# Kernel tuning notes

Measured on AMD Instinct MI355X. Metric: run time of the kernel, lower is better.

The kernel has to match this reference:

```python
import jax, jax.numpy as jnp
import numpy as np

B, M, C, S, SD, K, H = 32, 448, 384, 512, 128, 8, 8
DH = C // H
EPS = 1e-5
NEG_SLOPE = 0.2


def setup_inputs() -> dict:
    key = jax.random.key(0)
    ks = iter(jax.random.split(key, 32))
    nrm = lambda shape, scale=0.05: (jax.random.normal(next(ks), shape, jnp.float32) * scale)
    inp = {
        'q': jax.random.normal(next(ks), (B, M, C), jnp.float32),
        'coarse': jax.random.normal(next(ks), (B, M, 3), jnp.float32),
        'skeleton': jax.random.normal(next(ks), (B, S, 3), jnp.float32),
        # GraphConv 1: 3 -> 64 (root weight, rel/neighbor weight, bias)
        'gc1_wroot': nrm((3, 64), 0.3), 'gc1_wrel': nrm((3, 64), 0.3), 'gc1_b': jnp.zeros((64,), jnp.float32),
        # GraphConv 2: 64 -> SD
        'gc2_wroot': nrm((64, SD), 0.1), 'gc2_wrel': nrm((64, SD), 0.1), 'gc2_b': jnp.zeros((SD,), jnp.float32),
        # skeleton_projection: SD -> C
        'proj_w': nrm((SD, C), 0.08), 'proj_b': jnp.zeros((C,), jnp.float32),
        # MultiheadAttention (torch layout: in_proj (3C, C), out_proj (C, C))
        'attn_in_w': nrm((3 * C, C), 0.05), 'attn_in_b': jnp.zeros((3 * C,), jnp.float32),
        'attn_out_w': nrm((C, C), 0.05), 'attn_out_b': jnp.zeros((C,), jnp.float32),
        # increase_dim: Conv1d(C,1024,1) + BN(1024) + LeakyReLU + Conv1d(1024,1024,1)
        'inc1_w': nrm((1024, C), 0.05), 'inc1_b': jnp.zeros((1024,), jnp.float32),
        'bn_g': jnp.ones((1024,), jnp.float32), 'bn_b': jnp.zeros((1024,), jnp.float32),
        'bn_m': jnp.zeros((1024,), jnp.float32), 'bn_v': jnp.ones((1024,), jnp.float32),
        'inc2_w': nrm((1024, 1024), 0.03), 'inc2_b': jnp.zeros((1024,), jnp.float32),
        # reduce_map: Linear(C + 1024 + 3, C)
        'red_w': nrm((1024 + C + 3, C), 0.03), 'red_b': jnp.zeros((C,), jnp.float32),
    }
    return inp


def _knn_idx(pts):
    # pts: [B,S,3]; per-batch kNN (self excluded), matching knn_graph(k=K, batch=...)
    d2 = jnp.sum((pts[:, :, None, :] - pts[:, None, :, :]) ** 2, axis=-1)  # [B,S,S]
    d2 = d2 + jnp.eye(S, dtype=pts.dtype)[None] * 1e10                       # mask self
    _, idx = jax.lax.top_k(-d2, K)                                           # [B,S,K]
    return idx


def _graph_conv(x, idx, wroot, wrel, b):
    # GraphConv (PyG, aggr='add'): out_i = x_i Wroot + (sum_{j in N(i)} x_j) Wrel + b
    nb = jax.vmap(lambda f, i: f[i])(x, idx)   # [B,S,K,F]
    agg = nb.sum(axis=2)                       # [B,S,F]
    return x @ wroot + agg @ wrel + b


def reference(q, coarse, skeleton, gc1_wroot, gc1_wrel, gc1_b, gc2_wroot, gc2_wrel, gc2_b,
              proj_w, proj_b, attn_in_w, attn_in_b, attn_out_w, attn_out_b,
              inc1_w, inc1_b, bn_g, bn_b, bn_m, bn_v, inc2_w, inc2_b, red_w, red_b):
    # --- skeleton branch: knn graph + 2-layer GraphConv + max-pool + projection ---
    idx = _knn_idx(skeleton)
    h = _graph_conv(skeleton, idx, gc1_wroot, gc1_wrel, gc1_b)
    h = jax.nn.relu(h)
    h = _graph_conv(h, idx, gc2_wroot, gc2_wrel, gc2_b)        # [B,S,SD]
    proxy = jnp.max(h, axis=1)                                  # [B,SD]
    proxy = proxy @ proj_w + proj_b                             # [B,C]
    kv = jnp.broadcast_to(proxy[:, None, :], (B, M, C))         # expanded proxies

    # --- cross attention (torch nn.MultiheadAttention math) ---
    wq, wk, wv = attn_in_w[:C], attn_in_w[C:2 * C], attn_in_w[2 * C:]
    bq, bk, bv = attn_in_b[:C], attn_in_b[C:2 * C], attn_in_b[2 * C:]
    qh = (q @ wq.T + bq).reshape(B, M, H, DH)
    kh = (kv @ wk.T + bk).reshape(B, M, H, DH)
    vh = (kv @ wv.T + bv).reshape(B, M, H, DH)
    scores = jnp.einsum('bmhd,bnhd->bhmn', qh, kh) / jnp.sqrt(jnp.float32(DH))
    attn = jax.nn.softmax(scores, axis=-1)
    ctx = jnp.einsum('bhmn,bnhd->bmhd', attn, vh).reshape(B, M, C)
    q = ctx @ attn_out_w.T + attn_out_b                         # fused features [B,M,C]

    # --- increase_dim (1x1 conv == matmul) + BN(eval) + LeakyReLU + 1x1 conv ---
    g = jnp.einsum('bmc,oc->bmo', q, inc1_w) + inc1_b           # [B,M,1024]
    g = bn_g * (g - bn_m) * jax.lax.rsqrt(bn_v + EPS) + bn_b
    g = jnp.where(g >= 0, g, NEG_SLOPE * g)
    g = jnp.einsum('bmc,oc->bmo', g, inc2_w) + inc2_b
    global_feature = jnp.max(g, axis=1)                         # [B,1024]

    # --- concat + reduce_map ---
    rebuild = jnp.concatenate([jnp.broadcast_to(global_feature[:, None, :], (B, M, 1024)), q, coarse], axis=-1)
    out = rebuild @ red_w + red_b                               # [B,M,C]
    return out
```

## Files before the change

kernel.cpp:

```cpp
#include <hip/hip_runtime.h>

#define NB 32
#define MM 448
#define CC 384
#define SS 512
#define KNN 8
#define NBLK 512u

#define WS_IDX    0u
#define WS_H1     524288u
#define WS_PMAX   4718592u
#define WS_VV     4980736u
#define WS_Y      5029888u
#define WS_XCAT   5160960u
#define WS_BASEP  5341184u
#define WS_BAR    5390336u

#define AGENT __HIP_MEMORY_SCOPE_AGENT

__device__ __forceinline__ float ldg_f(const float* p) {
  return __hip_atomic_load(p, __ATOMIC_RELAXED, AGENT);
}
__device__ __forceinline__ void stg_f(float* p, float v) {
  __hip_atomic_store(p, v, __ATOMIC_RELAXED, AGENT);
}

__device__ __forceinline__ float wave_sum(float v) {
#pragma unroll
  for (int m = 1; m < 64; m <<= 1) v += __shfl_xor(v, m, 64);
  return v;
}

__device__ __forceinline__ void gbar(unsigned* bar, int phase, int blk) {
  asm volatile("s_waitcnt vmcnt(0)" ::: "memory");
  __syncthreads();
  if (threadIdx.x == 0) {
    __hip_atomic_fetch_add(bar + (blk & 7) * 16, 1u, __ATOMIC_RELAXED, AGENT);
    long spins = 0;
    unsigned tgt = (unsigned)(phase + 1);
    if (blk == 0) {
      unsigned target = NBLK * tgt;
      for (;;) {
        unsigned s = 0;
#pragma unroll
        for (int i = 0; i < 8; i++)
          s += __hip_atomic_load(bar + i * 16, __ATOMIC_RELAXED, AGENT);
        if (s >= target) break;
        __builtin_amdgcn_s_sleep(8);
        if (++spins > (1L << 21)) break;
      }
      __hip_atomic_store(bar + 8 * 16, tgt, __ATOMIC_RELAXED, AGENT);
    } else {
      while (__hip_atomic_load(bar + 8 * 16, __ATOMIC_RELAXED, AGENT) < tgt) {
        __builtin_amdgcn_s_sleep(8);
        if (++spins > (1L << 21)) break;
      }
    }
  }
  __syncthreads();
}

__global__ __launch_bounds__(256) void k_knn_gc1(
    const float* __restrict__ skel,
    const float* __restrict__ w1root, const float* __restrict__ w1rel,
    const float* __restrict__ b1,
    int* __restrict__ idx_ws, float* __restrict__ h1_ws,
    unsigned* __restrict__ bar)
{
  if (blockIdx.x == 0 && threadIdx.x < 9) bar[threadIdx.x * 16] = 0u;

  int b   = blockIdx.x >> 7;
  int grp = blockIdx.x & 127;
  __shared__ __align__(16) float4 sk[SS];
  const float* sb = skel + b * SS * 3;
  for (int t = threadIdx.x; t < SS; t += 256)
    sk[t] = make_float4(sb[t*3+0], sb[t*3+1], sb[t*3+2], 0.f);
  __syncthreads();

  int wave = threadIdx.x >> 6, lane = threadIdx.x & 63;
  int i = grp * 4 + wave;
  float4 pi = sk[i];

  float bd[KNN];
#pragma unroll
  for (int t = 0; t < KNN; t++) {
    int j = lane + (t << 6);
    float4 p = sk[j];
    float d2;
    {
#pragma clang fp contract(off)
      float dx = pi.x - p.x, dy = pi.y - p.y, dz = pi.z - p.z;
      d2 = (dx*dx + dy*dy) + dz*dz;
    }
    bd[t] = (j == i) ? 3e38f : d2;
  }

  int win[KNN];
  int* idx_base = idx_ws + (size_t)(b*SS + i) * KNN;
#pragma unroll
  for (int t = 0; t < KNN; t++) {
    float bestd = bd[0]; int bests = 0;
#pragma unroll
    for (int s = 1; s < KNN; s++)
      if (bd[s] < bestd) { bestd = bd[s]; bests = s; }
    int bestj = lane + (bests << 6);
#pragma unroll
    for (int m = 1; m < 64; m <<= 1) {
      float od = __shfl_xor(bestd, m, 64);
      int   oj = __shfl_xor(bestj, m, 64);
      if (od < bestd || (od == bestd && oj < bestj)) { bestd = od; bestj = oj; }
    }
    win[t] = bestj;
    if (lane == t) idx_base[t] = bestj;
    if ((bestj & 63) == lane) {
      int sl = bestj >> 6;
#pragma unroll
      for (int s = 0; s < KNN; s++) if (s == sl) bd[s] = 3e38f;
    }
  }

  float a0 = 0.f, a1 = 0.f, a2 = 0.f;
#pragma unroll
  for (int t = 0; t < KNN; t++) {
    float4 n = sk[win[t]];
    a0 += n.x; a1 += n.y; a2 += n.z;
  }

  int c = lane;
  float h = b1[c] + pi.x*w1root[c] + pi.y*w1root[64+c] + pi.z*w1root[128+c]
                  + a0*w1rel[c]   + a1*w1rel[64+c]   + a2*w1rel[128+c];
  h = fmaxf(h, 0.f);
  h1_ws[(size_t)(b*SS + i) * 64 + lane] = h;
}

struct CoopArgs {
  const float* h1; const int* idx;
  const float *g2wr, *g2wl, *g2b;
  const float *projw, *projb;
  const float *aiw, *aib, *aow, *aob;
  const float *i1w, *i1b, *bng, *bnb, *bnm, *bnv;
  const float *i2w, *i2b;
  const float *redw, *redb;
  const float* coarse;
  float *pmax, *vv, *y, *xcat, *basep, *out;
  unsigned* bar;
};

__global__ __launch_bounds__(256, 2) void k_fused(CoopArgs a)
{
  __shared__ __align__(16) float smem[9600];
  const int t   = threadIdx.x;
  const int blk = blockIdx.x;

  {
    int b = blk >> 4, chunk = blk & 15;
    int r0 = chunk * 32;
    float* X    = smem;
    float* Wt   = smem + 4128;
    float* mred = smem + 8224;
    int*   nbs  = (int*)(smem + 9248);

    const float* h1b = a.h1 + (size_t)b * SS * 64;
    nbs[t] = a.idx[(b*SS + r0)*KNN + t];
#pragma unroll
    for (int p = 0; p < 8; p++) {
      int idx = t + 256*p;
      int r = idx >> 6, k = idx & 63;
      X[r*129 + k] = h1b[(r0 + r)*64 + k];
    }
    __syncthreads();
#pragma unroll
    for (int p = 0; p < 8; p++) {
      int idx = t + 256*p;
      int r = idx >> 6, k = idx & 63;
      const int* nb = nbs + r*KNN;
      float s = 0.f;
#pragma unroll
      for (int j = 0; j < KNN; j++) s += h1b[nb[j]*64 + k];
      X[r*129 + 64 + k] = s;
    }

    int rg = t >> 5, cgi = t & 31;
    float acc[4][4];
#pragma unroll
    for (int r = 0; r < 4; r++)
#pragma unroll
      for (int u = 0; u < 4; u++) acc[r][u] = 0.f;

    const float* wsrc[4] = { a.g2wr, a.g2wr + 32*128, a.g2wl, a.g2wl + 32*128 };
#pragma unroll 1
    for (int ch = 0; ch < 4; ch++) {
      __syncthreads();
      const float* ws = wsrc[ch];
#pragma unroll
      for (int p = 0; p < 16; p++) {
        int idx = t + 256*p;
        Wt[idx] = ws[idx];
      }
      __syncthreads();
      int kb = ch * 32;
      const float* xr0 = X + (rg*4+0)*129 + kb;
      const float* xr1 = X + (rg*4+1)*129 + kb;
      const float* xr2 = X + (rg*4+2)*129 + kb;
      const float* xr3 = X + (rg*4+3)*129 + kb;
#pragma unroll 4
      for (int k = 0; k < 32; k++) {
        float4 w4 = *(const float4*)(Wt + k*128 + cgi*4);
        float x0 = xr0[k], x1 = xr1[k], x2 = xr2[k], x3 = xr3[k];
        acc[0][0] += x0*w4.x; acc[0][1] += x0*w4.y; acc[0][2] += x0*w4.z; acc[0][3] += x0*w4.w;
        acc[1][0] += x1*w4.x; acc[1][1] += x1*w4.y; acc[1][2] += x1*w4.z; acc[1][3] += x1*w4.w;
        acc[2][0] += x2*w4.x; acc[2][1] += x2*w4.y; acc[2][2] += x2*w4.z; acc[2][3] += x2*w4.w;
        acc[3][0] += x3*w4.x; acc[3][1] += x3*w4.y; acc[3][2] += x3*w4.z; acc[3][3] += x3*w4.w;
      }
    }
#pragma unroll
    for (int u = 0; u < 4; u++)
      mred[rg*128 + cgi*4 + u] =
        fmaxf(fmaxf(acc[0][u], acc[1][u]), fmaxf(acc[2][u], acc[3][u]));
    __syncthreads();
    if (t < 128) {
      float mx = mred[t];
#pragma unroll
      for (int g = 1; g < 8; g++) mx = fmaxf(mx, mred[g*128 + t]);
      stg_f(&a.pmax[(size_t)(b*16 + chunk)*128 + t], mx + a.g2b[t]);
    }
  }
  gbar(a.bar, 0, blk);

  if (blk < 384) {
    int b = blk & 31, og = blk >> 5;
    if (t < 128) {
      float m = -3e38f;
      for (int ch = 0; ch < 16; ch++)
        m = fmaxf(m, ldg_f(&a.pmax[(size_t)(b*16 + ch)*128 + t]));
      smem[t] = m;
    }
    __syncthreads();
    for (int o = t; o < CC; o += 256) {
      float acc = a.projb[o];
      for (int s = 0; s < 128; s++) acc += smem[s] * a.projw[s*CC + o];
      smem[128 + o] = acc;
    }
    __syncthreads();
    const float* xs = smem + 128;
    int wv = t >> 6, lane = t & 63;
    float x0 = xs[lane*6+0], x1 = xs[lane*6+1], x2 = xs[lane*6+2];
    float x3 = xs[lane*6+3], x4 = xs[lane*6+4], x5 = xs[lane*6+5];
#pragma unroll
    for (int u = 0; u < 8; u++) {
      int o = og*32 + wv*8 + u;
      const float* wr = a.aiw + (size_t)(2*CC + o) * CC + lane*6;
      float2 wa = *(const float2*)wr;
      float2 wb = *(const float2*)(wr + 2);
      float2 wc = *(const float2*)(wr + 4);
      float p = wa.x*x0 + wa.y*x1 + wb.x*x2 + wb.y*x3 + wc.x*x4 + wc.y*x5;
      p = wave_sum(p);
      if (lane == 0) stg_f(&a.vv[b*CC + o], a.aib[2*CC + o] + p);
    }
  }
  gbar(a.bar, 1, blk);

  if (blk < 384) {
    int b = blk & 31, og = blk >> 5;
    for (int i = t; i < CC; i += 256) smem[i] = ldg_f(&a.vv[b*CC + i]);
    __syncthreads();
    int wv = t >> 6, lane = t & 63;
    float x0 = smem[lane*6+0], x1 = smem[lane*6+1], x2 = smem[lane*6+2];
    float x3 = smem[lane*6+3], x4 = smem[lane*6+4], x5 = smem[lane*6+5];
#pragma unroll
    for (int u = 0; u < 8; u++) {
      int o = og*32 + wv*8 + u;
      const float* wr = a.aow + (size_t)o * CC + lane*6;
      float2 wa = *(const float2*)wr;
      float2 wb = *(const float2*)(wr + 2);
      float2 wc = *(const float2*)(wr + 4);
      float p = wa.x*x0 + wa.y*x1 + wb.x*x2 + wb.y*x3 + wc.x*x4 + wc.y*x5;
      p = wave_sum(p);
      if (lane == 0) stg_f(&a.xcat[b*1408 + 1024 + o], a.aob[o] + p);
    }
  }
  gbar(a.bar, 2, blk);

  {
    int b = blk >> 4, og = blk & 15;
    int o = og*64 + (t >> 2), qq = t & 3;
    for (int i = t; i < CC; i += 256) smem[i] = ldg_f(&a.xcat[b*1408 + 1024 + i]);
    __syncthreads();
    const float* wr = a.i1w + (size_t)o * CC + qq*96;
    const float* xr = smem + qq*96;
    float acc = 0.f;
#pragma unroll
    for (int kk = 0; kk < 96; kk += 4) {
      float4 w4 = *(const float4*)(wr + kk);
      float4 x4 = *(const float4*)(xr + kk);
      acc += w4.x*x4.x + w4.y*x4.y + w4.z*x4.z + w4.w*x4.w;
    }
    acc += __shfl_xor(acc, 1, 64);
    acc += __shfl_xor(acc, 2, 64);
    if (qq == 0) {
      float v = acc + a.i1b[o];
      float z = a.bng[o] * (v - a.bnm[o]) * rsqrtf(a.bnv[o] + 1e-5f) + a.bnb[o];
      stg_f(&a.y[b*1024 + o], (z >= 0.f) ? z : 0.2f * z);
    }
  }
  gbar(a.bar, 3, blk);

  {
    int b = blk >> 4, og = blk & 15;
    int o = og*64 + (t >> 2), qq = t & 3;
    for (int i = t; i < 1024; i += 256) smem[i] = ldg_f(&a.y[b*1024 + i]);
    __syncthreads();
    const float* wr = a.i2w + (size_t)o * 1024 + qq*256;
    const float* xr = smem + qq*256;
    float acc = 0.f;
#pragma unroll 8
    for (int kk = 0; kk < 256; kk += 4) {
      float4 w4 = *(const float4*)(wr + kk);
      float4 x4 = *(const float4*)(xr + kk);
      acc += w4.x*x4.x + w4.y*x4.y + w4.z*x4.z + w4.w*x4.w;
    }
    acc += __shfl_xor(acc, 1, 64);
    acc += __shfl_xor(acc, 2, 64);
    if (qq == 0) stg_f(&a.xcat[b*1408 + o], acc + a.i2b[o]);
  }
  gbar(a.bar, 4, blk);

  if (blk < 48) {
    int o0 = blk * 8;
    float* xs = smem;
    float* wt = smem + 4128;
    int o4 = t & 1, bb = (t >> 1) & 31, kq = t >> 6;
    float acc0 = 0.f, acc1 = 0.f, acc2 = 0.f, acc3 = 0.f;
#pragma unroll 1
    for (int c0 = 0; c0 < 1408; c0 += 128) {
      __syncthreads();
#pragma unroll
      for (int p = 0; p < 16; p++) {
        int idx = t + 256*p;
        xs[(idx >> 7)*129 + (idx & 127)] =
          ldg_f(&a.xcat[(idx >> 7)*1408 + c0 + (idx & 127)]);
      }
#pragma unroll
      for (int p = 0; p < 4; p++) {
        int idx = t + 256*p;
        wt[idx] = a.redw[(size_t)(c0 + (idx >> 3)) * CC + o0 + (idx & 7)];
      }
      __syncthreads();
      const float* xrow = xs + bb*129 + kq*32;
      const float* wrow = wt + kq*32*8 + o4*4;
#pragma unroll 8
      for (int i = 0; i < 32; i++) {
        float  x  = xrow[i];
        float4 w4 = *(const float4*)(wrow + i*8);
        acc0 += x*w4.x; acc1 += x*w4.y; acc2 += x*w4.z; acc3 += x*w4.w;
      }
    }
    __syncthreads();
    float* red = smem;
    red[t*4+0] = acc0; red[t*4+1] = acc1; red[t*4+2] = acc2; red[t*4+3] = acc3;
    __syncthreads();
    {
      int bb2 = t >> 3, oj = t & 7;
      float s = 0.f;
#pragma unroll
      for (int k2 = 0; k2 < 4; k2++)
        s += red[(k2*64 + bb2*2 + (oj >> 2))*4 + (oj & 3)];
      stg_f(&a.basep[bb2*CC + o0 + oj], s);
    }
  }
  gbar(a.bar, 5, blk);

  {
    int b = blk >> 4, mg = blk & 15;
    for (int i = t; i < CC; i += 256) smem[i] = ldg_f(&a.basep[b*CC + i]);
    __syncthreads();
    const int m0 = mg * 28;
    for (int i = t; i < 28*96; i += 256) {
      int mr = i / 96, c4 = i - mr*96;
      int row = b*MM + m0 + mr;
      int c = c4 * 4;
      float4 p0 = *(const float4*)(smem + c);
      float4 rb = *(const float4*)(a.redb + c);
      const float* cr = a.coarse + (size_t)row * 3;
      float cx = cr[0], cy = cr[1], cz = cr[2];
      float4 w0 = *(const float4*)(a.redw + (size_t)1408*CC + c);
      float4 w1 = *(const float4*)(a.redw + (size_t)1409*CC + c);
      float4 w2 = *(const float4*)(a.redw + (size_t)1410*CC + c);
      float4 o4v;
      o4v.x = p0.x + rb.x + cx*w0.x + cy*w1.x + cz*w2.x;
      o4v.y = p0.y + rb.y + cx*w0.y + cy*w1.y + cz*w2.y;
      o4v.z = p0.z + rb.z + cx*w0.z + cy*w1.z + cz*w2.z;
      o4v.w = p0.w + rb.w + cx*w0.w + cy*w1.w + cz*w2.w;
      *(float4*)(a.out + (size_t)row*CC + c) = o4v;
    }
  }
}

extern "C" void kernel_launch(void* const* d_in, const int* in_sizes, int n_in,
                              void* d_out, int out_size, void* d_ws, size_t ws_size,
                              hipStream_t stream)
{
  (void)in_sizes; (void)n_in; (void)out_size; (void)ws_size;
  const float* coarse = (const float*)d_in[1];
  const float* skel   = (const float*)d_in[2];
  const float* g1wr   = (const float*)d_in[3];
  const float* g1wl   = (const float*)d_in[4];
  const float* g1b    = (const float*)d_in[5];

  char* ws = (char*)d_ws;
  int*      idx_ws = (int*)(ws + WS_IDX);
  float*    h1_ws  = (float*)(ws + WS_H1);
  unsigned* bar    = (unsigned*)(ws + WS_BAR);

  CoopArgs a;
  a.h1    = h1_ws;
  a.idx   = idx_ws;
  a.g2wr  = (const float*)d_in[6];
  a.g2wl  = (const float*)d_in[7];
  a.g2b   = (const float*)d_in[8];
  a.projw = (const float*)d_in[9];
  a.projb = (const float*)d_in[10];
  a.aiw   = (const float*)d_in[11];
  a.aib   = (const float*)d_in[12];
  a.aow   = (const float*)d_in[13];
  a.aob   = (const float*)d_in[14];
  a.i1w   = (const float*)d_in[15];
  a.i1b   = (const float*)d_in[16];
  a.bng   = (const float*)d_in[17];
  a.bnb   = (const float*)d_in[18];
  a.bnm   = (const float*)d_in[19];
  a.bnv   = (const float*)d_in[20];
  a.i2w   = (const float*)d_in[21];
  a.i2b   = (const float*)d_in[22];
  a.redw  = (const float*)d_in[23];
  a.redb  = (const float*)d_in[24];
  a.coarse= coarse;
  a.pmax  = (float*)(ws + WS_PMAX);
  a.vv    = (float*)(ws + WS_VV);
  a.y     = (float*)(ws + WS_Y);
  a.xcat  = (float*)(ws + WS_XCAT);
  a.basep = (float*)(ws + WS_BASEP);
  a.out   = (float*)d_out;
  a.bar   = bar;

  k_knn_gc1<<<4096, 256, 0, stream>>>(skel, g1wr, g1wl, g1b, idx_ws, h1_ws, bar);
  k_fused<<<NBLK, 256, 0, stream>>>(a);
}
```

Baseline: 279.2 us.

## Restructure post-graph matvec phases across fewer blocks with decentralized grid barrier

Reworks the persistent kernel's grid barrier so every block polls the summed counters directly, instead of waiting for block 0 to publish a release flag, and uses thread fences instead of a raw waitcnt. The skeleton projection is now computed once by 32 blocks and stored to a new workspace buffer, replacing the redundant per-block recomputation. The attention V/out-projection and the two increase_dim matvecs now run on 48 or 128 blocks, each thread handling one (batch, output) pair with a float4 dot product, instead of all blocks sharing work through wave and shuffle reductions. This adds one more grid barrier and concentrates weight reads onto fewer blocks, which trades parallelism for less redundant work. It also replaces atomic loads with plain loads, relying on the fences for visibility.

```diff
diff --git a/kernel.cpp b/kernel.cpp
--- a/kernel.cpp
+++ b/kernel.cpp
@@ -10,54 +10,38 @@
 #define WS_IDX    0u
 #define WS_H1     524288u
 #define WS_PMAX   4718592u
-#define WS_VV     4980736u
-#define WS_Y      5029888u
-#define WS_XCAT   5160960u
-#define WS_BASEP  5341184u
-#define WS_BAR    5390336u
+#define WS_KV     4980736u
+#define WS_VV     5029888u
+#define WS_Y      5079040u
+#define WS_XCAT   5210112u
+#define WS_BASEP  5390336u
+#define WS_BAR    5439488u
 
 #define AGENT __HIP_MEMORY_SCOPE_AGENT
 
-__device__ __forceinline__ float ldg_f(const float* p) {
-  return __hip_atomic_load(p, __ATOMIC_RELAXED, AGENT);
-}
 __device__ __forceinline__ void stg_f(float* p, float v) {
   __hip_atomic_store(p, v, __ATOMIC_RELAXED, AGENT);
 }
 
-__device__ __forceinline__ float wave_sum(float v) {
-#pragma unroll
-  for (int m = 1; m < 64; m <<= 1) v += __shfl_xor(v, m, 64);
-  return v;
-}
-
 __device__ __forceinline__ void gbar(unsigned* bar, int phase, int blk) {
-  asm volatile("s_waitcnt vmcnt(0)" ::: "memory");
+  __threadfence();
   __syncthreads();
   if (threadIdx.x == 0) {
-    __hip_atomic_fetch_add(bar + (blk & 7) * 16, 1u, __ATOMIC_RELAXED, AGENT);
+    __hip_atomic_fetch_add(bar + (blk & 7) * 32, 1u, __ATOMIC_RELAXED, AGENT);
+    const unsigned target = NBLK * (unsigned)(phase + 1);
     long spins = 0;
-    unsigned tgt = (unsigned)(phase + 1);
-    if (blk == 0) {
-      unsigned target = NBLK * tgt;
-      for (;;) {
-        unsigned s = 0;
-#pragma unroll
-        for (int i = 0; i < 8; i++)
-          s += __hip_atomic_load(bar + i * 16, __ATOMIC_RELAXED, AGENT);
-        if (s >= target) break;
-        __builtin_amdgcn_s_sleep(8);
-        if (++spins > (1L << 21)) break;
-      }
-      __hip_atomic_store(bar + 8 * 16, tgt, __ATOMIC_RELAXED, AGENT);
-    } else {
-      while (__hip_atomic_load(bar + 8 * 16, __ATOMIC_RELAXED, AGENT) < tgt) {
-        __builtin_amdgcn_s_sleep(8);
-        if (++spins > (1L << 21)) break;
-      }
+    for (;;) {
+      unsigned s = 0;
+#pragma unroll
+      for (int i = 0; i < 8; i++)
+        s += __hip_atomic_load(bar + i * 32, __ATOMIC_RELAXED, AGENT);
+      if (s >= target) break;
+      __builtin_amdgcn_s_sleep(2);
+      if (++spins > (1L << 20)) break;
     }
   }
   __syncthreads();
+  __threadfence();
 }
 
 __global__ __launch_bounds__(256) void k_knn_gc1(
@@ -67,7 +51,7 @@
     int* __restrict__ idx_ws, float* __restrict__ h1_ws,
     unsigned* __restrict__ bar)
 {
-  if (blockIdx.x == 0 && threadIdx.x < 9) bar[threadIdx.x * 16] = 0u;
+  if (blockIdx.x == 0 && threadIdx.x < 8) bar[threadIdx.x * 32] = 0u;
 
   int b   = blockIdx.x >> 7;
   int grp = blockIdx.x & 127;
@@ -142,9 +126,25 @@
   const float *i2w, *i2b;
   const float *redw, *redb;
   const float* coarse;
-  float *pmax, *vv, *y, *xcat, *basep, *out;
+  float *pmax, *kv, *vv, *y, *xcat, *basep, *out;
   unsigned* bar;
 };
+
+__device__ __forceinline__ float matvec8(
+    const float* __restrict__ X, int xstride,
+    const float* __restrict__ Wrow, int wstride,
+    int o, int b, int K4)
+{
+  const float4* x4 = (const float4*)(X + (size_t)b * xstride);
+  const float4* w4 = (const float4*)(Wrow + (size_t)o * wstride);
+  float acc = 0.f;
+#pragma unroll 4
+  for (int k = 0; k < K4; k++) {
+    float4 xv = x4[k], wv = w4[k];
+    acc += xv.x*wv.x + xv.y*wv.y + xv.z*wv.z + xv.w*wv.w;
+  }
+  return acc;
+}
 
 __global__ __launch_bounds__(256, 2) void k_fused(CoopArgs a)
 {
@@ -227,103 +227,61 @@
   }
   gbar(a.bar, 0, blk);
 
-  if (blk < 384) {
-    int b = blk & 31, og = blk >> 5;
-    if (t < 128) {
+  if (blk < 32) {
+    int o0 = blk * 12;
+    float* proxy = smem;
+    for (int i = t; i < 4096; i += 256) {
+      int b = i >> 7, c = i & 127;
       float m = -3e38f;
+#pragma unroll 4
       for (int ch = 0; ch < 16; ch++)
-        m = fmaxf(m, ldg_f(&a.pmax[(size_t)(b*16 + ch)*128 + t]));
-      smem[t] = m;
-    }
-    __syncthreads();
-    for (int o = t; o < CC; o += 256) {
-      float acc = a.projb[o];
-      for (int s = 0; s < 128; s++) acc += smem[s] * a.projw[s*CC + o];
-      smem[128 + o] = acc;
-    }
-    __syncthreads();
-    const float* xs = smem + 128;
-    int wv = t >> 6, lane = t & 63;
-    float x0 = xs[lane*6+0], x1 = xs[lane*6+1], x2 = xs[lane*6+2];
-    float x3 = xs[lane*6+3], x4 = xs[lane*6+4], x5 = xs[lane*6+5];
-#pragma unroll
-    for (int u = 0; u < 8; u++) {
-      int o = og*32 + wv*8 + u;
-      const float* wr = a.aiw + (size_t)(2*CC + o) * CC + lane*6;
-      float2 wa = *(const float2*)wr;
-      float2 wb = *(const float2*)(wr + 2);
-      float2 wc = *(const float2*)(wr + 4);
-      float p = wa.x*x0 + wa.y*x1 + wb.x*x2 + wb.y*x3 + wc.x*x4 + wc.y*x5;
-      p = wave_sum(p);
-      if (lane == 0) stg_f(&a.vv[b*CC + o], a.aib[2*CC + o] + p);
+        m = fmaxf(m, a.pmax[(size_t)(b*16 + ch)*128 + c]);
+      proxy[b*129 + c] = m;
+    }
+    __syncthreads();
+#pragma unroll
+    for (int rep = 0; rep < 2; rep++) {
+      int p = t + rep*256;
+      if (p < 32*12) {
+        int b = p / 12, o = o0 + p % 12;
+        float acc = a.projb[o];
+        const float* pr = proxy + b*129;
+        for (int s = 0; s < 128; s++) acc += pr[s] * a.projw[s*CC + o];
+        stg_f(&a.kv[b*CC + o], acc);
+      }
     }
   }
   gbar(a.bar, 1, blk);
 
-  if (blk < 384) {
-    int b = blk & 31, og = blk >> 5;
-    for (int i = t; i < CC; i += 256) smem[i] = ldg_f(&a.vv[b*CC + i]);
-    __syncthreads();
-    int wv = t >> 6, lane = t & 63;
-    float x0 = smem[lane*6+0], x1 = smem[lane*6+1], x2 = smem[lane*6+2];
-    float x3 = smem[lane*6+3], x4 = smem[lane*6+4], x5 = smem[lane*6+5];
-#pragma unroll
-    for (int u = 0; u < 8; u++) {
-      int o = og*32 + wv*8 + u;
-      const float* wr = a.aow + (size_t)o * CC + lane*6;
-      float2 wa = *(const float2*)wr;
-      float2 wb = *(const float2*)(wr + 2);
-      float2 wc = *(const float2*)(wr + 4);
-      float p = wa.x*x0 + wa.y*x1 + wb.x*x2 + wb.y*x3 + wc.x*x4 + wc.y*x5;
-      p = wave_sum(p);
-      if (lane == 0) stg_f(&a.xcat[b*1408 + 1024 + o], a.aob[o] + p);
-    }
+  if (blk < 48) {
+    int o0 = blk * 8, b = t >> 3, o = o0 + (t & 7);
+    float acc = matvec8(a.kv, CC, a.aiw + (size_t)(2*CC)*CC, CC, o, b, CC/4);
+    stg_f(&a.vv[b*CC + o], acc + a.aib[2*CC + o]);
   }
   gbar(a.bar, 2, blk);
 
-  {
-    int b = blk >> 4, og = blk & 15;
-    int o = og*64 + (t >> 2), qq = t & 3;
-    for (int i = t; i < CC; i += 256) smem[i] = ldg_f(&a.xcat[b*1408 + 1024 + i]);
-    __syncthreads();
-    const float* wr = a.i1w + (size_t)o * CC + qq*96;
-    const float* xr = smem + qq*96;
-    float acc = 0.f;
-#pragma unroll
-    for (int kk = 0; kk < 96; kk += 4) {
-      float4 w4 = *(const float4*)(wr + kk);
-      float4 x4 = *(const float4*)(xr + kk);
-      acc += w4.x*x4.x + w4.y*x4.y + w4.z*x4.z + w4.w*x4.w;
-    }
-    acc += __shfl_xor(acc, 1, 64);
-    acc += __shfl_xor(acc, 2, 64);
-    if (qq == 0) {
-      float v = acc + a.i1b[o];
-      float z = a.bng[o] * (v - a.bnm[o]) * rsqrtf(a.bnv[o] + 1e-5f) + a.bnb[o];
-      stg_f(&a.y[b*1024 + o], (z >= 0.f) ? z : 0.2f * z);
-    }
+  if (blk < 48) {
+    int o0 = blk * 8, b = t >> 3, o = o0 + (t & 7);
+    float acc = matvec8(a.vv, CC, a.aow, CC, o, b, CC/4);
+    stg_f(&a.xcat[b*1408 + 1024 + o], acc + a.aob[o]);
   }
   gbar(a.bar, 3, blk);
 
-  {
-    int b = blk >> 4, og = blk & 15;
-    int o = og*64 + (t >> 2), qq = t & 3;
-    for (int i = t; i < 1024; i += 256) smem[i] = ldg_f(&a.y[b*1024 + i]);
-    __syncthreads();
-    const float* wr = a.i2w + (size_t)o * 1024 + qq*256;
-    const float* xr = smem + qq*256;
-    float acc = 0.f;
-#pragma unroll 8
-    for (int kk = 0; kk < 256; kk += 4) {
-      float4 w4 = *(const float4*)(wr + kk);
-      float4 x4 = *(const float4*)(xr + kk);
-      acc += w4.x*x4.x + w4.y*x4.y + w4.z*x4.z + w4.w*x4.w;
-    }
-    acc += __shfl_xor(acc, 1, 64);
-    acc += __shfl_xor(acc, 2, 64);
-    if (qq == 0) stg_f(&a.xcat[b*1408 + o], acc + a.i2b[o]);
+  if (blk < 128) {
+    int o0 = blk * 8, b = t >> 3, o = o0 + (t & 7);
+    float acc = matvec8(a.xcat + 1024, 1408, a.i1w, CC, o, b, CC/4);
+    float v = acc + a.i1b[o];
+    float z = a.bng[o] * (v - a.bnm[o]) * rsqrtf(a.bnv[o] + 1e-5f) + a.bnb[o];
+    stg_f(&a.y[b*1024 + o], (z >= 0.f) ? z : 0.2f * z);
   }
   gbar(a.bar, 4, blk);
+
+  if (blk < 128) {
+    int o0 = blk * 8, b = t >> 3, o = o0 + (t & 7);
+    float acc = matvec8(a.y, 1024, a.i2w, 1024, o, b, 1024/4);
+    stg_f(&a.xcat[b*1408 + o], acc + a.i2b[o]);
+  }
+  gbar(a.bar, 5, blk);
 
   if (blk < 48) {
     int o0 = blk * 8;
@@ -337,8 +295,7 @@
 #pragma unroll
       for (int p = 0; p < 16; p++) {
         int idx = t + 256*p;
-        xs[(idx >> 7)*129 + (idx & 127)] =
-          ldg_f(&a.xcat[(idx >> 7)*1408 + c0 + (idx & 127)]);
+        xs[(idx >> 7)*129 + (idx & 127)] = a.xcat[(idx >> 7)*1408 + c0 + (idx & 127)];
       }
 #pragma unroll
       for (int p = 0; p < 4; p++) {
@@ -368,11 +325,11 @@
       stg_f(&a.basep[bb2*CC + o0 + oj], s);
     }
   }
-  gbar(a.bar, 5, blk);
+  gbar(a.bar, 6, blk);
 
   {
     int b = blk >> 4, mg = blk & 15;
-    for (int i = t; i < CC; i += 256) smem[i] = ldg_f(&a.basep[b*CC + i]);
+    for (int i = t; i < CC; i += 256) smem[i] = a.basep[b*CC + i];
     __syncthreads();
     const int m0 = mg * 28;
     for (int i = t; i < 28*96; i += 256) {
@@ -436,6 +393,7 @@
   a.redb  = (const float*)d_in[24];
   a.coarse= coarse;
   a.pmax  = (float*)(ws + WS_PMAX);
+  a.kv    = (float*)(ws + WS_KV);
   a.vv    = (float*)(ws + WS_VV);
   a.y     = (float*)(ws + WS_Y);
   a.xcat  = (float*)(ws + WS_XCAT);
```

Result: slower. 792.2 us (+183.7%).
